# Kernel optimization log

Hardware: AMD Instinct MI355X
Metric: run time of the kernel (lower is better)

## Reference

```python
import jax, jax.numpy as jnp
import numpy as np

BN_EPS = 1e-5
NEG_SLOPE = 0.2


def _bn(h, gamma, beta, axes):
    # training-mode batch norm over given axes; channels on last axis
    mu = jnp.mean(h, axis=axes, keepdims=True)
    var = jnp.var(h, axis=axes, keepdims=True)
    return (h - mu) * jax.lax.rsqrt(var + BN_EPS) * gamma + beta


def _leaky(h):
    return jnp.where(h >= 0, h, NEG_SLOPE * h)


def setup_inputs() -> dict:
    key = jax.random.key(0)
    k0, k1, k2, k3 = jax.random.split(key, 4)
    B, N, C, K, M = 8, 1024, 512, 20, 64  # M = dim // downrate
    x = jax.random.normal(k0, (B, N, C), dtype=jnp.float32)
    idx = jax.random.randint(k1, (B, N, K), 0, N, dtype=jnp.int32)
    W1 = jax.random.normal(k2, (M, 2 * C), dtype=jnp.float32) * (1.0 / np.sqrt(2 * C))
    gamma1 = jnp.ones((M,), jnp.float32)
    beta1 = jnp.zeros((M,), jnp.float32)
    W2 = jax.random.normal(k3, (C, M), dtype=jnp.float32) * (1.0 / np.sqrt(M))
    gamma2 = jnp.ones((C,), jnp.float32)
    beta2 = jnp.zeros((C,), jnp.float32)
    return dict(x=x, idx=idx, W1=W1, gamma1=gamma1, beta1=beta1,
                W2=W2, gamma2=gamma2, beta2=beta2)


def reference(x, idx, W1, gamma1, beta1, W2, gamma2, beta2):
    # x: (B, N, C) point features; idx: (B, N, K) neighbor indices into N
    neigh = jax.vmap(lambda xb, ib: xb[ib])(x, idx)          # (B, N, K, C) gather
    center = x[:, :, None, :]                                 # (B, N, 1, C)
    # get_graph_feature: concat(feature - x, x) -> channels = 2C
    edge = jnp.concatenate(
        [neigh - center, jnp.broadcast_to(center, neigh.shape)], axis=-1)  # (B,N,K,2C)
    # conv1: 1x1 conv == per-edge linear, then BN2d (stats over B,N,K) + LeakyReLU
    h = jnp.einsum('bnkc,mc->bnkm', edge, W1)                 # (B, N, K, M)
    h = _leaky(_bn(h, gamma1, beta1, (0, 1, 2)))
    # max-aggregate over neighbors
    h = jnp.max(h, axis=2)                                    # (B, N, M)
    # conv2: 1x1 conv1d, BN1d (stats over B,N) + LeakyReLU
    h2 = jnp.einsum('bnm,dm->bnd', h, W2)                     # (B, N, C)
    h2 = _leaky(_bn(h2, gamma2, beta2, (0, 1)))
    return h2  # (B, N, dim), matches final permute(0, 2, 1)
```

## Files before the change

kernel.cpp:

```cpp
#include <hip/hip_runtime.h>
#include <math.h>

#define B_ 8
#define N_ 1024
#define C_ 512
#define K_ 20
#define M_ 64
#define R_ (B_*N_)

typedef short bf16x8 __attribute__((ext_vector_type(8)));
typedef float f32x4  __attribute__((ext_vector_type(4)));

#define WS_Y     0
#define WS_HMM   (WS_Y + R_*64)
#define WS_P1A   (WS_HMM + R_*64)
#define WS_P2A   (WS_P1A + 128)
#define WS_HB    (WS_P2A + 1024)
#define WS_W1B   (WS_HB + R_*32)
#define WS_W2B   (WS_W1B + 32768)

__device__ __forceinline__ uint f2b(float f) {
    union { float f; uint u; } v; v.f = f;
    return (v.u + 0x7fffu + ((v.u >> 16) & 1u)) >> 16;
}
__device__ __forceinline__ uint2 f4_to_b4(float4 v) {
    uint2 r;
    r.x = f2b(v.x) | (f2b(v.y) << 16);
    r.y = f2b(v.z) | (f2b(v.w) << 16);
    return r;
}
__device__ __forceinline__ float b2f(ushort u) {
    union { uint u; float f; } v; v.u = (uint)u << 16; return v.f;
}
__device__ __forceinline__ float bits2f(uint u) {
    union { uint u; float f; } v; v.u = u; return v.f;
}
__device__ __forceinline__ float lrelu(float v) { return v >= 0.f ? v : 0.2f * v; }

__global__ __launch_bounds__(256) void k_prep(const float* __restrict__ W1,
                                              const float* __restrict__ W2,
                                              ushort* __restrict__ W1b,
                                              ushort* __restrict__ W2b,
                                              float* __restrict__ P1a,
                                              float* __restrict__ P2a) {
    const int tid = blockIdx.x * 256 + threadIdx.x;
    if (tid < 8192) {
        const int o = tid * 8, j = o >> 9, k = o & 511;
        const float* src = (j < 64) ? &W1[(size_t)j * 1024 + k]
                                    : &W1[(size_t)(j - 64) * 1024 + 512 + k];
        const float4 a = *(const float4*)src;
        const float4 b = *(const float4*)(src + 4);
        const uint2 la = f4_to_b4(a), lb = f4_to_b4(b);
        uint4 v; v.x = la.x; v.y = la.y; v.z = lb.x; v.w = lb.y;
        ((uint4*)W1b)[tid] = v;
    } else if (tid < 12288) {
        const int t2 = tid - 8192, o = t2 * 8;
        const float4 a = *(const float4*)&W2[o];
        const float4 b = *(const float4*)&W2[o + 4];
        const uint2 la = f4_to_b4(a), lb = f4_to_b4(b);
        uint4 v; v.x = la.x; v.y = la.y; v.z = lb.x; v.w = lb.y;
        ((uint4*)W2b)[t2] = v;
    } else if (tid < 13312) {
        P2a[tid - 12288] = 0.f;
    } else if (tid < 13440) {
        P1a[tid - 13312] = 0.f;
    }
}

__global__ __launch_bounds__(256) void k_yz(const float* __restrict__ x,
                                            const ushort* __restrict__ W1b,
                                            ushort* __restrict__ Y) {
    __shared__ __align__(16) ushort sWb[65536];
    const int t = threadIdx.x, lane = t & 63, w = t >> 6;
    const int wr = w >> 1, wc = w & 1;
    const int r0 = blockIdx.x * 32;

#pragma unroll
    for (int i = 0; i < 32; ++i) {
        const int f = i * 256 + t;
        const int j = f >> 6, kq = f & 63;
        const uint4 v = ((const uint4*)W1b)[f];
        const int off = j * 1024 + ((kq * 16) ^ ((j & 7) << 4));
        *(uint4*)((char*)sWb + off) = v;
    }

    const int arow = r0 + wr * 16 + (lane & 15);
    const size_t xbase = (size_t)arow * 512 + ((lane >> 4) * 8);
    float4 xr[8][4];
#pragma unroll
    for (int ks = 0; ks < 8; ++ks) {
        const size_t b = xbase + ks * 64;
        xr[ks][0] = *(const float4*)&x[b];
        xr[ks][1] = *(const float4*)&x[b + 4];
        xr[ks][2] = *(const float4*)&x[b + 32];
        xr[ks][3] = *(const float4*)&x[b + 36];
    }

    f32x4 acc[4];
#pragma unroll
    for (int jj = 0; jj < 4; ++jj) acc[jj] = (f32x4){0.f, 0.f, 0.f, 0.f};

    __syncthreads();

    const int jbase = wc * 64 + (lane & 15);
    const int kb_base = (lane >> 4) * 16;

#pragma unroll
    for (int ks = 0; ks < 8; ++ks) {
        const uint2 c00 = f4_to_b4(xr[ks][0]), c01 = f4_to_b4(xr[ks][1]);
        const uint2 c10 = f4_to_b4(xr[ks][2]), c11 = f4_to_b4(xr[ks][3]);
        union { uint4 u; bf16x8 b; } A0, A1;
        A0.u.x = c00.x; A0.u.y = c00.y; A0.u.z = c01.x; A0.u.w = c01.y;
        A1.u.x = c10.x; A1.u.y = c10.y; A1.u.z = c11.x; A1.u.w = c11.y;
        const int k0 = ks * 128 + kb_base;
#pragma unroll
        for (int jj = 0; jj < 4; ++jj) {
            const int jrow = jbase + jj * 16;
            const int rowoff = jrow * 1024;
            const int sw = (jrow & 7) << 4;
            const bf16x8 B0 = *(const bf16x8*)((char*)sWb + rowoff + (k0 ^ sw));
            const bf16x8 B1 = *(const bf16x8*)((char*)sWb + rowoff + ((k0 + 64) ^ sw));
            acc[jj] = __builtin_amdgcn_mfma_f32_16x16x32_bf16(A0.b, B0, acc[jj], 0, 0, 0);
            acc[jj] = __builtin_amdgcn_mfma_f32_16x16x32_bf16(A1.b, B1, acc[jj], 0, 0, 0);
        }
    }

    const int crow = r0 + wr * 16 + (lane >> 4) * 4;
    const int ccol = wc * 64 + (lane & 15);
#pragma unroll
    for (int jj = 0; jj < 4; ++jj)
#pragma unroll
        for (int i = 0; i < 4; ++i)
            Y[(size_t)(crow + i) * 128 + ccol + jj * 16] = (ushort)f2b(acc[jj][i]);
}

__global__ __launch_bounds__(256) void k_gather(const ushort* __restrict__ Y,
                                                const int* __restrict__ idx,
                                                uint* __restrict__ HMM,
                                                float* __restrict__ P1a) {
    __shared__ float sRed[4][128];
    const int t = threadIdx.x;
    const int w = t >> 6, lane = t & 63;
    const int p0 = blockIdx.x * 16 + w * 4;
    float s_sum = 0.f, s_sq = 0.f;
#pragma unroll
    for (int i = 0; i < 4; ++i) {
        const int p = p0 + i;
        const int b = p >> 10;
        const float ys = b2f(Y[(size_t)p * 128 + lane]);
        const float zs = b2f(Y[(size_t)p * 128 + 64 + lane]);
        const float base = zs - ys;
        float hmx = -INFINITY, hmn = INFINITY;
        const int* ip = &idx[p * K_];
#pragma unroll
        for (int k = 0; k < K_; ++k) {
            const int j = ip[k];
            const float yg = b2f(Y[((size_t)(b * N_ + j)) * 128 + lane]);
            const float h = yg + base;
            s_sum += h;
            s_sq  += h * h;
            hmx = fmaxf(hmx, h);
            hmn = fminf(hmn, h);
        }
        HMM[(size_t)p * 64 + lane] = f2b(hmx) | (f2b(hmn) << 16);
    }
    sRed[w][lane]      = s_sum;
    sRed[w][64 + lane] = s_sq;
    __syncthreads();
    if (t < 128) {
        const float v = sRed[0][t] + sRed[1][t] + sRed[2][t] + sRed[3][t];
        atomicAdd(&P1a[t], v);
    }
}

__global__ __launch_bounds__(256) void k_qsum(const uint* __restrict__ HMM,
                                              const float* __restrict__ P1a,
                                              const float* __restrict__ g1,
                                              const float* __restrict__ b1,
                                              const ushort* __restrict__ W2b,
                                              ushort* __restrict__ Hb,
                                              float* __restrict__ P2a) {
    __shared__ float sSc1[64], sSh1[64];
    const int t = threadIdx.x, lane = t & 63, w = t >> 6;
    if (t < 64) {
        const float inv = 1.f / (float)(R_ * K_);
        const float mu  = P1a[t] * inv;
        const float var = P1a[64 + t] * inv - mu * mu;
        const float rs  = rsqrtf(var + 1e-5f);
        const float sc  = g1[t] * rs;
        sSc1[t] = sc;
        sSh1[t] = b1[t] - mu * sc;
    }
    __syncthreads();

    const int rtile = blockIdx.x, half = blockIdx.y;
    const int r0 = rtile * 64;
    const int dsub = half * 256 + w * 64;
    const int qd = lane >> 4, s = lane & 15;
    const int mc0 = qd * 8;

    bf16x8 bfr[4][2];
#pragma unroll
    for (int f = 0; f < 4; ++f)
#pragma unroll
        for (int g = 0; g < 2; ++g)
            bfr[f][g] = *(const bf16x8*)&W2b[(size_t)(dsub + f * 16 + s) * 64 + mc0 + g * 32];

    f32x4 acc[4][4];
#pragma unroll
    for (int rt = 0; rt < 4; ++rt)
#pragma unroll
        for (int f = 0; f < 4; ++f) acc[rt][f] = (f32x4){0.f,0.f,0.f,0.f};

#pragma unroll
    for (int rt = 0; rt < 4; ++rt) {
        const int row = r0 + rt * 16 + s;
#pragma unroll
        for (int g = 0; g < 2; ++g) {
            const int mc = mc0 + g * 32;
            const uint4 u0 = *(const uint4*)&HMM[(size_t)row * 64 + mc];
            const uint4 u1 = *(const uint4*)&HMM[(size_t)row * 64 + mc + 4];
            float v[8];
#pragma unroll
            for (int i = 0; i < 4; ++i) {
                const uint ua = ((const uint*)&u0)[i];
                const uint ub = ((const uint*)&u1)[i];
                const float c0 = sSc1[mc + i],     h0 = sSh1[mc + i];
                const float c4 = sSc1[mc + 4 + i], h4 = sSh1[mc + 4 + i];
                const float a0 = c0 >= 0.f ? bits2f(ua << 16) : bits2f(ua & 0xffff0000u);
                const float a4 = c4 >= 0.f ? bits2f(ub << 16) : bits2f(ub & 0xffff0000u);
                v[i]     = lrelu(a0 * c0 + h0);
                v[i + 4] = lrelu(a4 * c4 + h4);
            }
            uint4 pk;
            pk.x = f2b(v[0]) | (f2b(v[1]) << 16);
            pk.y = f2b(v[2]) | (f2b(v[3]) << 16);
            pk.z = f2b(v[4]) | (f2b(v[5]) << 16);
            pk.w = f2b(v[6]) | (f2b(v[7]) << 16);
            if (half == 0) *(uint4*)&Hb[(size_t)row * 64 + mc] = pk;
            union { uint4 u; bf16x8 b; } cv; cv.u = pk;
#pragma unroll
            for (int f = 0; f < 4; ++f)
                acc[rt][f] = __builtin_amdgcn_mfma_f32_16x16x32_bf16(cv.b, bfr[f][g], acc[rt][f], 0, 0, 0);
        }
    }

#pragma unroll
    for (int f = 0; f < 4; ++f) {
        float ss = 0.f, qq = 0.f;
#pragma unroll
        for (int rt = 0; rt < 4; ++rt)
#pragma unroll
            for (int i = 0; i < 4; ++i) {
                const float vv = acc[rt][f][i];
                ss += vv; qq += vv * vv;
            }
        ss += __shfl_xor(ss, 16); ss += __shfl_xor(ss, 32);
        qq += __shfl_xor(qq, 16); qq += __shfl_xor(qq, 32);
        if (lane < 16) {
            const int d = dsub + f * 16 + s;
            atomicAdd(&P2a[d], ss);
            atomicAdd(&P2a[512 + d], qq);
        }
    }
}

__global__ __launch_bounds__(256) void k_out(const ushort* __restrict__ Hb,
                                             const ushort* __restrict__ W2b,
                                             const float* __restrict__ P2a,
                                             const float* __restrict__ g2,
                                             const float* __restrict__ b2,
                                             float* __restrict__ out) {
    __shared__ float sSc2[256], sSh2[256];
    const int t = threadIdx.x, lane = t & 63, w = t >> 6;
    const int rtile = blockIdx.x, half = blockIdx.y;
    {
        const int d = half * 256 + t;
        const float inv = 1.f / (float)R_;
        const float mu  = P2a[d] * inv;
        const float var = P2a[512 + d] * inv - mu * mu;
        const float rs  = rsqrtf(var + 1e-5f);
        const float sc  = g2[d] * rs;
        sSc2[t] = sc;
        sSh2[t] = b2[d] - mu * sc;
    }
    __syncthreads();

    const int r0 = rtile * 64;
    const int dsub = half * 256 + w * 64;
    const int qd = lane >> 4, s = lane & 15;
    const int mc0 = qd * 8;

    bf16x8 bfr[4][2];
#pragma unroll
    for (int f = 0; f < 4; ++f)
#pragma unroll
        for (int g = 0; g < 2; ++g)
            bfr[f][g] = *(const bf16x8*)&W2b[(size_t)(dsub + f * 16 + s) * 64 + mc0 + g * 32];

    f32x4 acc[4][4];
#pragma unroll
    for (int rt = 0; rt < 4; ++rt)
#pragma unroll
        for (int f = 0; f < 4; ++f) acc[rt][f] = (f32x4){0.f,0.f,0.f,0.f};

#pragma unroll
    for (int rt = 0; rt < 4; ++rt) {
        const int row = r0 + rt * 16 + s;
#pragma unroll
        for (int g = 0; g < 2; ++g) {
            const bf16x8 af = *(const bf16x8*)&Hb[(size_t)row * 64 + mc0 + g * 32];
#pragma unroll
            for (int f = 0; f < 4; ++f)
                acc[rt][f] = __builtin_amdgcn_mfma_f32_16x16x32_bf16(af, bfr[f][g], acc[rt][f], 0, 0, 0);
        }
    }

#pragma unroll
    for (int rt = 0; rt < 4; ++rt)
#pragma unroll
        for (int f = 0; f < 4; ++f) {
            const int dl = w * 64 + f * 16 + s;
            const float c2 = sSc2[dl], h2 = sSh2[dl];
            const int d = dsub + f * 16 + s;
#pragma unroll
            for (int i = 0; i < 4; ++i) {
                const float vv = lrelu(acc[rt][f][i] * c2 + h2);
                out[(size_t)(r0 + rt * 16 + qd * 4 + i) * 512 + d] = vv;
            }
        }
}

extern "C" void kernel_launch(void* const* d_in, const int* in_sizes, int n_in,
                              void* d_out, int out_size, void* d_ws, size_t ws_size,
                              hipStream_t stream) {
    const float* x   = (const float*)d_in[0];
    const int*   idx = (const int*)d_in[1];
    const float* W1  = (const float*)d_in[2];
    const float* g1  = (const float*)d_in[3];
    const float* b1  = (const float*)d_in[4];
    const float* W2  = (const float*)d_in[5];
    const float* g2  = (const float*)d_in[6];
    const float* b2  = (const float*)d_in[7];
    float* out = (float*)d_out;
    float* ws  = (float*)d_ws;

    ushort* Y    = (ushort*)(ws + WS_Y);
    uint*   HMM  = (uint*)(ws + WS_HMM);
    float*  P1a  = ws + WS_P1A;
    float*  P2a  = ws + WS_P2A;
    ushort* Hb   = (ushort*)(ws + WS_HB);
    ushort* W1b  = (ushort*)(ws + WS_W1B);
    ushort* W2b  = (ushort*)(ws + WS_W2B);

    k_prep  <<<dim3(56),      dim3(256), 0, stream>>>(W1, W2, W1b, W2b, P1a, P2a);
    k_yz    <<<dim3(R_ / 32), dim3(256), 0, stream>>>(x, W1b, Y);
    k_gather<<<dim3(R_ / 16), dim3(256), 0, stream>>>(Y, idx, HMM, P1a);
    k_qsum  <<<dim3(128, 2),  dim3(256), 0, stream>>>(HMM, P1a, g1, b1, W2b, Hb, P2a);
    k_out   <<<dim3(128, 2),  dim3(256), 0, stream>>>(Hb, W2b, P2a, g2, b2, out);
}
```

Measured before the change: 51.61 us.

## Fuse weight prep into k_yz and merge qsum/out via cooperative grid sync

Removes the separate weight-conversion kernel: k_yz now converts W1 to bf16 straight into shared memory and zeroes the stat accumulators, and the second GEMM block converts W2 on the fly. The qsum and output kernels are merged into one cooperative kernel that keeps the GEMM accumulators in registers across a grid-wide sync, so the Hb intermediate buffer and the recomputed second GEMM disappear. This cuts two launches and some global traffic. In exchange, every k_yz block redundantly converts all of W1 from fp32, and the fused kernel pays for a cooperative launch and a grid barrier. It also relies on all 256 blocks being co-resident.

```diff
diff --git a/kernel.cpp b/kernel.cpp
--- a/kernel.cpp
+++ b/kernel.cpp
@@ -1,5 +1,8 @@
 #include <hip/hip_runtime.h>
+#include <hip/hip_cooperative_groups.h>
 #include <math.h>
+
+namespace cg = cooperative_groups;
 
 #define B_ 8
 #define N_ 1024
@@ -15,9 +18,6 @@
 #define WS_HMM   (WS_Y + R_*64)
 #define WS_P1A   (WS_HMM + R_*64)
 #define WS_P2A   (WS_P1A + 128)
-#define WS_HB    (WS_P2A + 1024)
-#define WS_W1B   (WS_HB + R_*32)
-#define WS_W2B   (WS_W1B + 32768)
 
 __device__ __forceinline__ uint f2b(float f) {
     union { float f; uint u; } v; v.f = f;
@@ -37,52 +37,31 @@
 }
 __device__ __forceinline__ float lrelu(float v) { return v >= 0.f ? v : 0.2f * v; }
 
-__global__ __launch_bounds__(256) void k_prep(const float* __restrict__ W1,
-                                              const float* __restrict__ W2,
-                                              ushort* __restrict__ W1b,
-                                              ushort* __restrict__ W2b,
-                                              float* __restrict__ P1a,
-                                              float* __restrict__ P2a) {
-    const int tid = blockIdx.x * 256 + threadIdx.x;
-    if (tid < 8192) {
-        const int o = tid * 8, j = o >> 9, k = o & 511;
-        const float* src = (j < 64) ? &W1[(size_t)j * 1024 + k]
-                                    : &W1[(size_t)(j - 64) * 1024 + 512 + k];
+__global__ __launch_bounds__(256) void k_yz(const float* __restrict__ x,
+                                            const float* __restrict__ W1,
+                                            ushort* __restrict__ Y,
+                                            float* __restrict__ P1a,
+                                            float* __restrict__ P2a) {
+    __shared__ __align__(16) ushort sWb[65536];
+    const int t = threadIdx.x, lane = t & 63, w = t >> 6;
+    const int wr = w >> 1, wc = w & 1;
+    const int r0 = blockIdx.x * 32;
+
+#pragma unroll 8
+    for (int i = 0; i < 32; ++i) {
+        const int f = i * 256 + t;
+        const int j = f >> 6, kq = f & 63;
+        const float* src = (j < 64) ? &W1[(size_t)j * 1024 + kq * 8]
+                                    : &W1[(size_t)(j - 64) * 1024 + 512 + kq * 8];
         const float4 a = *(const float4*)src;
         const float4 b = *(const float4*)(src + 4);
         const uint2 la = f4_to_b4(a), lb = f4_to_b4(b);
         uint4 v; v.x = la.x; v.y = la.y; v.z = lb.x; v.w = lb.y;
-        ((uint4*)W1b)[tid] = v;
-    } else if (tid < 12288) {
-        const int t2 = tid - 8192, o = t2 * 8;
-        const float4 a = *(const float4*)&W2[o];
-        const float4 b = *(const float4*)&W2[o + 4];
-        const uint2 la = f4_to_b4(a), lb = f4_to_b4(b);
-        uint4 v; v.x = la.x; v.y = la.y; v.z = lb.x; v.w = lb.y;
-        ((uint4*)W2b)[t2] = v;
-    } else if (tid < 13312) {
-        P2a[tid - 12288] = 0.f;
-    } else if (tid < 13440) {
-        P1a[tid - 13312] = 0.f;
-    }
-}
-
-__global__ __launch_bounds__(256) void k_yz(const float* __restrict__ x,
-                                            const ushort* __restrict__ W1b,
-                                            ushort* __restrict__ Y) {
-    __shared__ __align__(16) ushort sWb[65536];
-    const int t = threadIdx.x, lane = t & 63, w = t >> 6;
-    const int wr = w >> 1, wc = w & 1;
-    const int r0 = blockIdx.x * 32;
-
-#pragma unroll
-    for (int i = 0; i < 32; ++i) {
-        const int f = i * 256 + t;
-        const int j = f >> 6, kq = f & 63;
-        const uint4 v = ((const uint4*)W1b)[f];
         const int off = j * 1024 + ((kq * 16) ^ ((j & 7) << 4));
         *(uint4*)((char*)sWb + off) = v;
     }
+    if (blockIdx.x == 0 && t < 128) P1a[t] = 0.f;
+    if (blockIdx.x >= 1 && blockIdx.x <= 4) P2a[(blockIdx.x - 1) * 256 + t] = 0.f;
 
     const int arow = r0 + wr * 16 + (lane & 15);
     const size_t xbase = (size_t)arow * 512 + ((lane >> 4) * 8);
@@ -173,13 +152,16 @@
     }
 }
 
-__global__ __launch_bounds__(256) void k_qsum(const uint* __restrict__ HMM,
-                                              const float* __restrict__ P1a,
-                                              const float* __restrict__ g1,
-                                              const float* __restrict__ b1,
-                                              const ushort* __restrict__ W2b,
-                                              ushort* __restrict__ Hb,
-                                              float* __restrict__ P2a) {
+__global__ __launch_bounds__(256) void k_fused2(const uint* __restrict__ HMM,
+                                                const float* __restrict__ P1a,
+                                                const float* __restrict__ g1,
+                                                const float* __restrict__ b1,
+                                                const float* __restrict__ W2,
+                                                const float* __restrict__ g2,
+                                                const float* __restrict__ b2,
+                                                float* __restrict__ P2a,
+                                                float* __restrict__ out) {
+    cg::grid_group grid = cg::this_grid();
     __shared__ float sSc1[64], sSh1[64];
     const int t = threadIdx.x, lane = t & 63, w = t >> 6;
     if (t < 64) {
@@ -193,7 +175,7 @@
     }
     __syncthreads();
 
-    const int rtile = blockIdx.x, half = blockIdx.y;
+    const int rtile = blockIdx.x >> 1, half = blockIdx.x & 1;
     const int r0 = rtile * 64;
     const int dsub = half * 256 + w * 64;
     const int qd = lane >> 4, s = lane & 15;
@@ -201,10 +183,18 @@
 
     bf16x8 bfr[4][2];
 #pragma unroll
-    for (int f = 0; f < 4; ++f)
-#pragma unroll
-        for (int g = 0; g < 2; ++g)
-            bfr[f][g] = *(const bf16x8*)&W2b[(size_t)(dsub + f * 16 + s) * 64 + mc0 + g * 32];
+    for (int f = 0; f < 4; ++f) {
+        const int d = dsub + f * 16 + s;
+#pragma unroll
+        for (int g = 0; g < 2; ++g) {
+            const float4 wa = *(const float4*)&W2[(size_t)d * 64 + mc0 + g * 32];
+            const float4 wb = *(const float4*)&W2[(size_t)d * 64 + mc0 + g * 32 + 4];
+            const uint2 lo = f4_to_b4(wa), hi = f4_to_b4(wb);
+            union { uint4 u; bf16x8 b; } cv;
+            cv.u.x = lo.x; cv.u.y = lo.y; cv.u.z = hi.x; cv.u.w = hi.y;
+            bfr[f][g] = cv.b;
+        }
+    }
 
     f32x4 acc[4][4];
 #pragma unroll
@@ -237,7 +227,6 @@
             pk.y = f2b(v[2]) | (f2b(v[3]) << 16);
             pk.z = f2b(v[4]) | (f2b(v[5]) << 16);
             pk.w = f2b(v[6]) | (f2b(v[7]) << 16);
-            if (half == 0) *(uint4*)&Hb[(size_t)row * 64 + mc] = pk;
             union { uint4 u; bf16x8 b; } cv; cv.u = pk;
 #pragma unroll
             for (int f = 0; f < 4; ++f)
@@ -263,69 +252,29 @@
             atomicAdd(&P2a[512 + d], qq);
         }
     }
-}
-
-__global__ __launch_bounds__(256) void k_out(const ushort* __restrict__ Hb,
-                                             const ushort* __restrict__ W2b,
-                                             const float* __restrict__ P2a,
-                                             const float* __restrict__ g2,
-                                             const float* __restrict__ b2,
-                                             float* __restrict__ out) {
-    __shared__ float sSc2[256], sSh2[256];
-    const int t = threadIdx.x, lane = t & 63, w = t >> 6;
-    const int rtile = blockIdx.x, half = blockIdx.y;
-    {
-        const int d = half * 256 + t;
+    __threadfence();
+    grid.sync();
+
+    float c2[4], h2s[4];
+#pragma unroll
+    for (int f = 0; f < 4; ++f) {
+        const int d = dsub + f * 16 + s;
         const float inv = 1.f / (float)R_;
         const float mu  = P2a[d] * inv;
         const float var = P2a[512 + d] * inv - mu * mu;
         const float rs  = rsqrtf(var + 1e-5f);
         const float sc  = g2[d] * rs;
-        sSc2[t] = sc;
-        sSh2[t] = b2[d] - mu * sc;
-    }
-    __syncthreads();
-
-    const int r0 = rtile * 64;
-    const int dsub = half * 256 + w * 64;
-    const int qd = lane >> 4, s = lane & 15;
-    const int mc0 = qd * 8;
-
-    bf16x8 bfr[4][2];
-#pragma unroll
-    for (int f = 0; f < 4; ++f)
-#pragma unroll
-        for (int g = 0; g < 2; ++g)
-            bfr[f][g] = *(const bf16x8*)&W2b[(size_t)(dsub + f * 16 + s) * 64 + mc0 + g * 32];
-
-    f32x4 acc[4][4];
+        c2[f]  = sc;
+        h2s[f] = b2[d] - mu * sc;
+    }
 #pragma unroll
     for (int rt = 0; rt < 4; ++rt)
 #pragma unroll
-        for (int f = 0; f < 4; ++f) acc[rt][f] = (f32x4){0.f,0.f,0.f,0.f};
-
-#pragma unroll
-    for (int rt = 0; rt < 4; ++rt) {
-        const int row = r0 + rt * 16 + s;
-#pragma unroll
-        for (int g = 0; g < 2; ++g) {
-            const bf16x8 af = *(const bf16x8*)&Hb[(size_t)row * 64 + mc0 + g * 32];
-#pragma unroll
-            for (int f = 0; f < 4; ++f)
-                acc[rt][f] = __builtin_amdgcn_mfma_f32_16x16x32_bf16(af, bfr[f][g], acc[rt][f], 0, 0, 0);
-        }
-    }
-
-#pragma unroll
-    for (int rt = 0; rt < 4; ++rt)
-#pragma unroll
         for (int f = 0; f < 4; ++f) {
-            const int dl = w * 64 + f * 16 + s;
-            const float c2 = sSc2[dl], h2 = sSh2[dl];
             const int d = dsub + f * 16 + s;
 #pragma unroll
             for (int i = 0; i < 4; ++i) {
-                const float vv = lrelu(acc[rt][f][i] * c2 + h2);
+                const float vv = lrelu(acc[rt][f][i] * c2[f] + h2s[f]);
                 out[(size_t)(r0 + rt * 16 + qd * 4 + i) * 512 + d] = vv;
             }
         }
@@ -349,13 +298,13 @@
     uint*   HMM  = (uint*)(ws + WS_HMM);
     float*  P1a  = ws + WS_P1A;
     float*  P2a  = ws + WS_P2A;
-    ushort* Hb   = (ushort*)(ws + WS_HB);
-    ushort* W1b  = (ushort*)(ws + WS_W1B);
-    ushort* W2b  = (ushort*)(ws + WS_W2B);
-
-    k_prep  <<<dim3(56),      dim3(256), 0, stream>>>(W1, W2, W1b, W2b, P1a, P2a);
-    k_yz    <<<dim3(R_ / 32), dim3(256), 0, stream>>>(x, W1b, Y);
+
+    k_yz    <<<dim3(R_ / 32), dim3(256), 0, stream>>>(x, W1, Y, P1a, P2a);
     k_gather<<<dim3(R_ / 16), dim3(256), 0, stream>>>(Y, idx, HMM, P1a);
-    k_qsum  <<<dim3(128, 2),  dim3(256), 0, stream>>>(HMM, P1a, g1, b1, W2b, Hb, P2a);
-    k_out   <<<dim3(128, 2),  dim3(256), 0, stream>>>(Hb, W2b, P2a, g2, b2, out);
-}
+
+    void* args[] = {
+        (void*)&HMM, (void*)&P1a, (void*)&g1, (void*)&b1,
+        (void*)&W2, (void*)&g2, (void*)&b2, (void*)&P2a, (void*)&out
+    };
+    hipLaunchCooperativeKernel((void*)k_fused2, dim3(256), dim3(256), args, 0, stream);
+}
```

After: 95.36 us. 84.8% more time.

## Fold weight prep into consumer kernels and vectorize neighbor gather

Applied to the files above, without the earlier changes.

Removes the separate weight-conversion kernel. Each block of the first GEMM kernel now converts W1 from fp32 to bf16 directly into shared memory, and the second-stage kernels convert W2 in registers. Accumulator zeroing moves into the first kernel. The gather kernel is reworked so each lane handles two channels with 32-bit loads, idx is loaded as int4, and each block covers 32 points, halving the block count. This saves a launch and the intermediate weight buffers, at the cost of redundant per-block fp32 weight reads and conversion.

```diff
diff --git a/kernel.cpp b/kernel.cpp
--- a/kernel.cpp
+++ b/kernel.cpp
@@ -16,8 +16,6 @@
 #define WS_P1A   (WS_HMM + R_*64)
 #define WS_P2A   (WS_P1A + 128)
 #define WS_HB    (WS_P2A + 1024)
-#define WS_W1B   (WS_HB + R_*32)
-#define WS_W2B   (WS_W1B + 32768)
 
 __device__ __forceinline__ uint f2b(float f) {
     union { float f; uint u; } v; v.f = f;
@@ -29,60 +27,36 @@
     r.y = f2b(v.z) | (f2b(v.w) << 16);
     return r;
 }
-__device__ __forceinline__ float b2f(ushort u) {
-    union { uint u; float f; } v; v.u = (uint)u << 16; return v.f;
-}
 __device__ __forceinline__ float bits2f(uint u) {
     union { uint u; float f; } v; v.u = u; return v.f;
 }
 __device__ __forceinline__ float lrelu(float v) { return v >= 0.f ? v : 0.2f * v; }
 
-__global__ __launch_bounds__(256) void k_prep(const float* __restrict__ W1,
-                                              const float* __restrict__ W2,
-                                              ushort* __restrict__ W1b,
-                                              ushort* __restrict__ W2b,
-                                              float* __restrict__ P1a,
-                                              float* __restrict__ P2a) {
-    const int tid = blockIdx.x * 256 + threadIdx.x;
-    if (tid < 8192) {
-        const int o = tid * 8, j = o >> 9, k = o & 511;
-        const float* src = (j < 64) ? &W1[(size_t)j * 1024 + k]
-                                    : &W1[(size_t)(j - 64) * 1024 + 512 + k];
+__global__ __launch_bounds__(256) void k_yz(const float* __restrict__ x,
+                                            const float* __restrict__ W1,
+                                            ushort* __restrict__ Y,
+                                            float* __restrict__ P1a,
+                                            float* __restrict__ P2a) {
+    __shared__ __align__(16) ushort sWb[65536];
+    const int t = threadIdx.x, lane = t & 63, w = t >> 6;
+    const int wr = w >> 1, wc = w & 1;
+    const int r0 = blockIdx.x * 32;
+
+#pragma unroll 8
+    for (int i = 0; i < 32; ++i) {
+        const int f = i * 256 + t;
+        const int j = f >> 6, kq = f & 63;
+        const float* src = (j < 64) ? &W1[(size_t)j * 1024 + kq * 8]
+                                    : &W1[(size_t)(j - 64) * 1024 + 512 + kq * 8];
         const float4 a = *(const float4*)src;
         const float4 b = *(const float4*)(src + 4);
         const uint2 la = f4_to_b4(a), lb = f4_to_b4(b);
         uint4 v; v.x = la.x; v.y = la.y; v.z = lb.x; v.w = lb.y;
-        ((uint4*)W1b)[tid] = v;
-    } else if (tid < 12288) {
-        const int t2 = tid - 8192, o = t2 * 8;
-        const float4 a = *(const float4*)&W2[o];
-        const float4 b = *(const float4*)&W2[o + 4];
-        const uint2 la = f4_to_b4(a), lb = f4_to_b4(b);
-        uint4 v; v.x = la.x; v.y = la.y; v.z = lb.x; v.w = lb.y;
-        ((uint4*)W2b)[t2] = v;
-    } else if (tid < 13312) {
-        P2a[tid - 12288] = 0.f;
-    } else if (tid < 13440) {
-        P1a[tid - 13312] = 0.f;
-    }
-}
-
-__global__ __launch_bounds__(256) void k_yz(const float* __restrict__ x,
-                                            const ushort* __restrict__ W1b,
-                                            ushort* __restrict__ Y) {
-    __shared__ __align__(16) ushort sWb[65536];
-    const int t = threadIdx.x, lane = t & 63, w = t >> 6;
-    const int wr = w >> 1, wc = w & 1;
-    const int r0 = blockIdx.x * 32;
-
-#pragma unroll
-    for (int i = 0; i < 32; ++i) {
-        const int f = i * 256 + t;
-        const int j = f >> 6, kq = f & 63;
-        const uint4 v = ((const uint4*)W1b)[f];
         const int off = j * 1024 + ((kq * 16) ^ ((j & 7) << 4));
         *(uint4*)((char*)sWb + off) = v;
     }
+    if (blockIdx.x == 0 && t < 128) P1a[t] = 0.f;
+    if (blockIdx.x >= 1 && blockIdx.x <= 4) P2a[(blockIdx.x - 1) * 256 + t] = 0.f;
 
     const int arow = r0 + wr * 16 + (lane & 15);
     const size_t xbase = (size_t)arow * 512 + ((lane >> 4) * 8);
@@ -138,38 +112,52 @@
                                                 const int* __restrict__ idx,
                                                 uint* __restrict__ HMM,
                                                 float* __restrict__ P1a) {
-    __shared__ float sRed[4][128];
-    const int t = threadIdx.x;
-    const int w = t >> 6, lane = t & 63;
-    const int p0 = blockIdx.x * 16 + w * 4;
-    float s_sum = 0.f, s_sq = 0.f;
-#pragma unroll
-    for (int i = 0; i < 4; ++i) {
-        const int p = p0 + i;
-        const int b = p >> 10;
-        const float ys = b2f(Y[(size_t)p * 128 + lane]);
-        const float zs = b2f(Y[(size_t)p * 128 + 64 + lane]);
-        const float base = zs - ys;
-        float hmx = -INFINITY, hmn = INFINITY;
-        const int* ip = &idx[p * K_];
-#pragma unroll
-        for (int k = 0; k < K_; ++k) {
-            const int j = ip[k];
-            const float yg = b2f(Y[((size_t)(b * N_ + j)) * 128 + lane]);
-            const float h = yg + base;
-            s_sum += h;
-            s_sq  += h * h;
-            hmx = fmaxf(hmx, h);
-            hmn = fminf(hmn, h);
-        }
-        HMM[(size_t)p * 64 + lane] = f2b(hmx) | (f2b(hmn) << 16);
-    }
-    sRed[w][lane]      = s_sum;
-    sRed[w][64 + lane] = s_sq;
+    __shared__ float sSum[8][64];
+    __shared__ float sQ[8][64];
+    const int t = threadIdx.x, lane = t & 63, w = t >> 6;
+    const int sub = lane >> 5, c = lane & 31;
+    const int grp = w * 2 + sub;
+    const uint* Yu = (const uint*)Y;
+    float sum0 = 0.f, sum1 = 0.f, sq0 = 0.f, sq1 = 0.f;
+
+#pragma unroll
+    for (int pi = 0; pi < 4; ++pi) {
+        const int p = blockIdx.x * 32 + w * 8 + pi * 2 + sub;
+        const int bb = p >> 10;
+        const uint ysu = Yu[(size_t)p * 64 + c];
+        const uint zsu = Yu[(size_t)p * 64 + 32 + c];
+        const float base0 = bits2f(zsu << 16) - bits2f(ysu << 16);
+        const float base1 = bits2f(zsu & 0xffff0000u) - bits2f(ysu & 0xffff0000u);
+        float mx0 = -INFINITY, mx1 = -INFINITY, mn0 = INFINITY, mn1 = INFINITY;
+        int4 j4[5];
+#pragma unroll
+        for (int q = 0; q < 5; ++q) j4[q] = *(const int4*)&idx[p * 20 + q * 4];
+#pragma unroll
+        for (int k = 0; k < 20; ++k) {
+            const int j = ((const int*)j4)[k];
+            const uint yg = Yu[(size_t)(bb * 1024 + j) * 64 + c];
+            const float h0 = bits2f(yg << 16) + base0;
+            const float h1 = bits2f(yg & 0xffff0000u) + base1;
+            sum0 += h0; sum1 += h1;
+            sq0 += h0 * h0; sq1 += h1 * h1;
+            mx0 = fmaxf(mx0, h0); mx1 = fmaxf(mx1, h1);
+            mn0 = fminf(mn0, h0); mn1 = fminf(mn1, h1);
+        }
+        uint2 st;
+        st.x = f2b(mx0) | (f2b(mn0) << 16);
+        st.y = f2b(mx1) | (f2b(mn1) << 16);
+        *(uint2*)&HMM[(size_t)p * 64 + 2 * c] = st;
+    }
+
+    *(float2*)&sSum[grp][2 * c] = make_float2(sum0, sum1);
+    *(float2*)&sQ[grp][2 * c]   = make_float2(sq0, sq1);
     __syncthreads();
-    if (t < 128) {
-        const float v = sRed[0][t] + sRed[1][t] + sRed[2][t] + sRed[3][t];
-        atomicAdd(&P1a[t], v);
+    if (t < 64) {
+        float s = 0.f, q = 0.f;
+#pragma unroll
+        for (int g = 0; g < 8; ++g) { s += sSum[g][t]; q += sQ[g][t]; }
+        atomicAdd(&P1a[t], s);
+        atomicAdd(&P1a[64 + t], q);
     }
 }
 
@@ -177,7 +165,7 @@
                                               const float* __restrict__ P1a,
                                               const float* __restrict__ g1,
                                               const float* __restrict__ b1,
-                                              const ushort* __restrict__ W2b,
+                                              const float* __restrict__ W2,
                                               ushort* __restrict__ Hb,
                                               float* __restrict__ P2a) {
     __shared__ float sSc1[64], sSh1[64];
@@ -201,10 +189,18 @@
 
     bf16x8 bfr[4][2];
 #pragma unroll
-    for (int f = 0; f < 4; ++f)
-#pragma unroll
-        for (int g = 0; g < 2; ++g)
-            bfr[f][g] = *(const bf16x8*)&W2b[(size_t)(dsub + f * 16 + s) * 64 + mc0 + g * 32];
+    for (int f = 0; f < 4; ++f) {
+        const int d = dsub + f * 16 + s;
+#pragma unroll
+        for (int g = 0; g < 2; ++g) {
+            const float4 wa = *(const float4*)&W2[(size_t)d * 64 + mc0 + g * 32];
+            const float4 wb = *(const float4*)&W2[(size_t)d * 64 + mc0 + g * 32 + 4];
+            const uint2 lo = f4_to_b4(wa), hi = f4_to_b4(wb);
+            union { uint4 u; bf16x8 b; } cv;
+            cv.u.x = lo.x; cv.u.y = lo.y; cv.u.z = hi.x; cv.u.w = hi.y;
+            bfr[f][g] = cv.b;
+        }
+    }
 
     f32x4 acc[4][4];
 #pragma unroll
@@ -266,7 +262,7 @@
 }
 
 __global__ __launch_bounds__(256) void k_out(const ushort* __restrict__ Hb,
-                                             const ushort* __restrict__ W2b,
+                                             const float* __restrict__ W2,
                                              const float* __restrict__ P2a,
                                              const float* __restrict__ g2,
                                              const float* __restrict__ b2,
@@ -293,10 +289,18 @@
 
     bf16x8 bfr[4][2];
 #pragma unroll
-    for (int f = 0; f < 4; ++f)
-#pragma unroll
-        for (int g = 0; g < 2; ++g)
-            bfr[f][g] = *(const bf16x8*)&W2b[(size_t)(dsub + f * 16 + s) * 64 + mc0 + g * 32];
+    for (int f = 0; f < 4; ++f) {
+        const int d = dsub + f * 16 + s;
+#pragma unroll
+        for (int g = 0; g < 2; ++g) {
+            const float4 wa = *(const float4*)&W2[(size_t)d * 64 + mc0 + g * 32];
+            const float4 wb = *(const float4*)&W2[(size_t)d * 64 + mc0 + g * 32 + 4];
+            const uint2 lo = f4_to_b4(wa), hi = f4_to_b4(wb);
+            union { uint4 u; bf16x8 b; } cv;
+            cv.u.x = lo.x; cv.u.y = lo.y; cv.u.z = hi.x; cv.u.w = hi.y;
+            bfr[f][g] = cv.b;
+        }
+    }
 
     f32x4 acc[4][4];
 #pragma unroll
@@ -350,12 +354,9 @@
     float*  P1a  = ws + WS_P1A;
     float*  P2a  = ws + WS_P2A;
     ushort* Hb   = (ushort*)(ws + WS_HB);
-    ushort* W1b  = (ushort*)(ws + WS_W1B);
-    ushort* W2b  = (ushort*)(ws + WS_W2B);
-
-    k_prep  <<<dim3(56),      dim3(256), 0, stream>>>(W1, W2, W1b, W2b, P1a, P2a);
-    k_yz    <<<dim3(R_ / 32), dim3(256), 0, stream>>>(x, W1b, Y);
-    k_gather<<<dim3(R_ / 16), dim3(256), 0, stream>>>(Y, idx, HMM, P1a);
-    k_qsum  <<<dim3(128, 2),  dim3(256), 0, stream>>>(HMM, P1a, g1, b1, W2b, Hb, P2a);
-    k_out   <<<dim3(128, 2),  dim3(256), 0, stream>>>(Hb, W2b, P2a, g2, b2, out);
-}
+
+    k_yz    <<<dim3(R_ / 32), dim3(256), 0, stream>>>(x, W1, Y, P1a, P2a);
+    k_gather<<<dim3(R_ / 32), dim3(256), 0, stream>>>(Y, idx, HMM, P1a);
+    k_qsum  <<<dim3(128, 2),  dim3(256), 0, stream>>>(HMM, P1a, g1, b1, W2, Hb, P2a);
+    k_out   <<<dim3(128, 2),  dim3(256), 0, stream>>>(Hb, W2, P2a, g2, b2, out);
+}
```

New measurement: 52.32 us. No clear change (+1.4%).
